# Kernel tuning notes

Hardware: AMD Instinct MI355X
Metric: run time of the kernel (lower is better)

Reference implementation:

```python
import jax, jax.numpy as jnp
import numpy as np

B, S, D, H, E = 4, 1024, 1024, 4096, 8


def setup_inputs() -> dict:
    key = jax.random.key(0)
    ks = jax.random.split(key, 5)
    sd = 1.0 / np.sqrt(D)
    sh = 1.0 / np.sqrt(H)
    x = jax.random.normal(ks[0], (B, S, D), dtype=jnp.float32)
    # stacked expert weights: Linear(D->H), ReLU, Linear(H->D)
    W1 = jax.random.normal(ks[1], (E, D, H), dtype=jnp.float32) * sd
    b1 = jnp.zeros((E, H), dtype=jnp.float32)
    W2 = jax.random.normal(ks[2], (E, H, D), dtype=jnp.float32) * sh
    b2 = jnp.zeros((E, D), dtype=jnp.float32)
    # gate Linear(D->E)
    Wg = jax.random.normal(ks[3], (D, E), dtype=jnp.float32) * sd
    bg = jnp.zeros((E,), dtype=jnp.float32)
    return {"x": x, "W1": W1, "b1": b1, "W2": W2, "b2": b2,
            "Wg": Wg, "bg": bg, "top_k": 2}


def reference(x, W1, b1, W2, b2, Wg, bg, top_k):
    # gating
    gating_scores = jnp.einsum('bsd,de->bse', x, Wg) + bg          # [B,S,E]
    gating_probs = jax.nn.softmax(gating_scores, axis=-1)
    _, top_k_indices = jax.lax.top_k(gating_probs, top_k)          # [B,S,K]
    n_exp = Wg.shape[1]
    # per-token 0/1 mask of selected experts (matches torch sum over k of mask)
    # NOTE: original code multiplies by the binary mask only; top_k_probs are
    # computed but NOT used as combine weights. We reproduce that faithfully.
    sel = jnp.sum(top_k_indices[..., None] == jnp.arange(n_exp), axis=2)  # [B,S,E]
    sel = sel.astype(x.dtype)
    # dense all-experts FFN (as the original does)
    h = jax.nn.relu(jnp.einsum('bsd,edh->bseh', x, W1) + b1)       # [B,S,E,H]
    eo = jnp.einsum('bseh,ehd->bsed', h, W2) + b2                  # [B,S,E,D]
    output = jnp.einsum('bsed,bse->bsd', eo, sel)                  # [B,S,D]
    return (output, gating_scores)
```

## Files before the change

### kernel.cpp

```cpp
#include <hip/hip_runtime.h>
#include <hip/hip_bf16.h>
#include <stdint.h>

#define B_ 4
#define S_ 1024
#define D_ 1024
#define H_ 4096
#define E_ 8
#define T_ (B_*S_)

#define BM 256
#define BN 256
#define BK 64
#define MAXT1 640
#define MAXT2 320

typedef __bf16 bf16x8 __attribute__((ext_vector_type(8)));
typedef float f32x4 __attribute__((ext_vector_type(4)));
typedef unsigned short ushort8 __attribute__((ext_vector_type(8)));

__device__ __forceinline__ unsigned short f2bf(float f) {
  union { float f; uint32_t u; } v; v.f = f;
  uint32_t u = v.u;
  u += 0x7fff + ((u >> 16) & 1);
  return (unsigned short)(u >> 16);
}

__device__ __forceinline__ void gl16(const void* g, void* l) {
  __builtin_amdgcn_global_load_lds(
      (const __attribute__((address_space(1))) void*)g,
      (__attribute__((address_space(3))) void*)l,
      16, 0, 0);
}
#define MEMFENCE asm volatile("" ::: "memory")

__global__ __launch_bounds__(256) void conv_x_kernel(
    const float* __restrict__ x, unsigned short* __restrict__ xb) {
  size_t i = ((size_t)blockIdx.x * 256 + threadIdx.x) * 8;
  const float4* s = (const float4*)(x + i);
  float4 v0 = s[0], v1 = s[1];
  ushort8 w;
  w[0]=f2bf(v0.x); w[1]=f2bf(v0.y); w[2]=f2bf(v0.z); w[3]=f2bf(v0.w);
  w[4]=f2bf(v1.x); w[5]=f2bf(v1.y); w[6]=f2bf(v1.z); w[7]=f2bf(v1.w);
  *(ushort8*)(xb + i) = w;
}

__global__ __launch_bounds__(256) void transpose_conv(
    const float* __restrict__ in, unsigned short* __restrict__ outp,
    int R, int C) {
  __shared__ float tile[64][68];
  const int e = blockIdx.z;
  const size_t eoff = (size_t)e * R * C;
  const int r0 = blockIdx.y * 64, c0 = blockIdx.x * 64;
  const int t = threadIdx.x;
  {
    const int r = t >> 2, cq = (t & 3) * 16;
    const float4* s4 = (const float4*)(in + eoff + (size_t)(r0 + r) * C + (c0 + cq));
#pragma unroll
    for (int i = 0; i < 4; ++i)
      *(float4*)&tile[r][cq + i * 4] = s4[i];
  }
  __syncthreads();
  {
    const int c = t >> 2, r8 = (t & 3) * 16;
    unsigned short* dst = outp + eoff + (size_t)(c0 + c) * R + (r0 + r8);
    ushort8 w0, w1;
#pragma unroll
    for (int j = 0; j < 8; ++j) {
      w0[j] = f2bf(tile[r8 + j][c]);
      w1[j] = f2bf(tile[r8 + 8 + j][c]);
    }
    *(ushort8*)dst = w0;
    *(ushort8*)(dst + 8) = w1;
  }
}

__global__ __launch_bounds__(256) void gating_kernel(
    const float* __restrict__ x, const float* __restrict__ Wg,
    const float* __restrict__ bg, float* __restrict__ scores,
    int* __restrict__ cnt, int* __restrict__ lists) {
  int t = blockIdx.x * 4 + (threadIdx.x >> 6);
  int l = threadIdx.x & 63;
  float acc[E_];
#pragma unroll
  for (int e = 0; e < E_; ++e) acc[e] = 0.f;
  const float* xr = x + (size_t)t * D_;
  for (int k = l; k < D_; k += 64) {
    float xv = xr[k];
    const float4* w = (const float4*)(Wg + (size_t)k * E_);
    float4 w0 = w[0], w1 = w[1];
    acc[0] += xv * w0.x; acc[1] += xv * w0.y; acc[2] += xv * w0.z; acc[3] += xv * w0.w;
    acc[4] += xv * w1.x; acc[5] += xv * w1.y; acc[6] += xv * w1.z; acc[7] += xv * w1.w;
  }
#pragma unroll
  for (int off = 32; off > 0; off >>= 1)
#pragma unroll
    for (int e = 0; e < E_; ++e) acc[e] += __shfl_xor(acc[e], off, 64);
  if (l == 0) {
    float s[E_];
#pragma unroll
    for (int e = 0; e < E_; ++e) {
      s[e] = acc[e] + bg[e];
      scores[(size_t)t * E_ + e] = s[e];
    }
    int i1 = 0; float m1 = -1e30f;
#pragma unroll
    for (int e = 0; e < E_; ++e) if (s[e] > m1) { m1 = s[e]; i1 = e; }
    int i2 = -1; float m2 = -1e30f;
#pragma unroll
    for (int e = 0; e < E_; ++e) if (e != i1 && s[e] > m2) { m2 = s[e]; i2 = e; }
    int p1 = atomicAdd(&cnt[i1], 1); lists[i1 * T_ + p1] = t;
    int p2 = atomicAdd(&cnt[i2], 1); lists[i2 * T_ + p2] = t;
  }
}

__global__ void scan_kernel(const int* __restrict__ cnt, int* __restrict__ off,
                            int* __restrict__ hdr, int* __restrict__ t1tab,
                            int* __restrict__ t2tab) {
  if (threadIdx.x == 0) {
    int o = 0;
    int mtiles[E_];
    for (int e = 0; e < E_; ++e) {
      off[e] = o; o += cnt[e];
      mtiles[e] = (cnt[e] + BM - 1) / BM;
    }
    int n1 = 0;
    for (int e = 0; e < E_; ++e)
      for (int g = 0; g < 4; ++g)
        for (int mt = 0; mt < mtiles[e]; ++mt)
          for (int nl = 0; nl < 4; ++nl)
            t1tab[n1++] = (e << 20) | (mt << 8) | (g * 4 + nl);
    int n2 = 0;
    for (int e = 0; e < E_; ++e)
      for (int sp = 0; sp < 2; ++sp)
        for (int mt = 0; mt < mtiles[e]; ++mt)
          for (int nt = 0; nt < 4; ++nt)
            t2tab[n2++] = (e << 20) | (mt << 8) | (sp << 4) | nt;
    hdr[0] = n1; hdr[1] = n2;
  }
}

template <int LAYER, int SPLITK>
__global__ __launch_bounds__(512, 2) void ffn_gemm(
    const unsigned short* __restrict__ xb,
    const unsigned short* __restrict__ hbuf,
    const unsigned short* __restrict__ WT,
    const float* __restrict__ bias,
    const int* __restrict__ cnt, const int* __restrict__ off,
    const int* __restrict__ lists,
    const int* __restrict__ tab, const int* __restrict__ hdr,
    unsigned short* __restrict__ hout,
    float* __restrict__ out)
{
  constexpr int K = (LAYER == 1) ? D_ : H_;
  constexpr int N = (LAYER == 1) ? H_ : D_;
  constexpr int KS = K / SPLITK;
  constexpr int NT = KS / BK;

  const int ntask = hdr[LAYER - 1];
  const int b = blockIdx.x;
  if (b >= ntask) return;
  const int q = ntask >> 3, r = ntask & 7;
  const int x = b & 7, ii = b >> 3;
  const int task = (x < r ? x * (q + 1) : r * (q + 1) + (x - r) * q) + ii;

  const int ent = tab[task];
  const int e  = ent >> 20;
  const int m0 = ((ent >> 8) & 0xff) * BM;
  const int sp = (ent >> 4) & 3;
  const int n0 = (ent & 15) * BN;
  const int k0 = sp * KS;
  const int count = cnt[e];
  const int oe = off[e];
  const int* lst = lists + e * T_;

  __shared__ unsigned short sA[2][BM * BK];
  __shared__ unsigned short sB[2][BN * BK];

  const int tid  = threadIdx.x;
  const int lane = tid & 63;
  const int wv   = tid >> 6;
  const int wm   = (wv >> 2) * 128;
  const int wn   = (wv & 3) * 64;

  const int srow   = lane >> 3;
  const int schunk = (lane & 7) * 16;
  const int sgoff  = schunk ^ (srow << 4);

  const char* arow[4];
  const char* brow[4];
#pragma unroll
  for (int i = 0; i < 4; ++i) {
    int rr = i * 64 + wv * 8 + srow;
    int gr = m0 + rr;
    if (LAYER == 1) {
      int tok = (gr < count) ? lst[gr] : lst[m0];
      arow[i] = (const char*)(xb + (size_t)tok * K + k0);
    } else {
      int r2 = (gr < count) ? gr : m0;
      arow[i] = (const char*)(hbuf + (size_t)(oe + r2) * K + k0);
    }
    brow[i] = (const char*)(WT + (size_t)e * N * K + (size_t)(n0 + rr) * K + k0);
  }

  auto stage = [&](int buf, int t) {
    const int kb = t * 128;
#pragma unroll
    for (int i = 0; i < 4; ++i)
      gl16(arow[i] + kb + sgoff, (char*)&sA[buf][0] + (i * 64 + wv * 8) * 128);
#pragma unroll
    for (int i = 0; i < 4; ++i)
      gl16(brow[i] + kb + sgoff, (char*)&sB[buf][0] + (i * 64 + wv * 8) * 128);
  };

  const int lrow = lane & 15;
  const int kg   = lane >> 4;
  const int fswz = (lrow & 7) << 4;

  f32x4 acc[8][4];
#pragma unroll
  for (int i = 0; i < 8; ++i)
#pragma unroll
    for (int j = 0; j < 4; ++j) acc[i][j] = (f32x4){0.f, 0.f, 0.f, 0.f};

  stage(0, 0);
  stage(1, 1);
  asm volatile("s_waitcnt vmcnt(8)" ::: "memory");
  __builtin_amdgcn_s_barrier();
  MEMFENCE;

  for (int t = 0; t < NT; ++t) {
    const int buf = t & 1;
    bf16x8 af[8][2], bfm[4][2];
#pragma unroll
    for (int i = 0; i < 8; ++i) {
      const int ra = wm + i * 16 + lrow;
#pragma unroll
      for (int ks = 0; ks < 2; ++ks)
        af[i][ks] = *(const bf16x8*)((const char*)&sA[buf][0] + ra * 128 + ((ks * 64 + kg * 16) ^ fswz));
    }
#pragma unroll
    for (int j = 0; j < 4; ++j) {
      const int rb = wn + j * 16 + lrow;
#pragma unroll
      for (int ks = 0; ks < 2; ++ks)
        bfm[j][ks] = *(const bf16x8*)((const char*)&sB[buf][0] + rb * 128 + ((ks * 64 + kg * 16) ^ fswz));
    }
    MEMFENCE;
    __builtin_amdgcn_s_barrier();
    MEMFENCE;
    if (t + 2 < NT) stage(buf, t + 2);
    __builtin_amdgcn_s_setprio(1);
#pragma unroll
    for (int ks = 0; ks < 2; ++ks)
#pragma unroll
      for (int i = 0; i < 8; ++i)
#pragma unroll
        for (int j = 0; j < 4; ++j)
          acc[i][j] = __builtin_amdgcn_mfma_f32_16x16x32_bf16(af[i][ks], bfm[j][ks], acc[i][j], 0, 0, 0);
    __builtin_amdgcn_s_setprio(0);
    if (t + 2 < NT) {
      asm volatile("s_waitcnt vmcnt(8)" ::: "memory");
    } else if (t + 1 < NT) {
      asm volatile("s_waitcnt vmcnt(0)" ::: "memory");
    }
    MEMFENCE;
    __builtin_amdgcn_s_barrier();
    MEMFENCE;
  }

  const int rbase = 4 * kg;
#pragma unroll
  for (int i = 0; i < 8; ++i) {
#pragma unroll
    for (int r2 = 0; r2 < 4; ++r2) {
      int row  = wm + i * 16 + rbase + r2;
      int grow = m0 + row;
      if (grow < count) {
#pragma unroll
        for (int j = 0; j < 4; ++j) {
          int col  = wn + j * 16 + lrow;
          int gcol = n0 + col;
          float bv = (SPLITK == 1 || sp == 0) ? bias[(size_t)e * N + gcol] : 0.f;
          float v = acc[i][j][r2] + bv;
          if (LAYER == 1) {
            v = v > 0.f ? v : 0.f;
            hout[(size_t)(oe + grow) * H_ + gcol] = f2bf(v);
          } else {
            int tok = lst[grow];
            atomicAdd(&out[(size_t)tok * D_ + gcol], v);
          }
        }
      }
    }
  }
}

extern "C" void kernel_launch(void* const* d_in, const int* in_sizes, int n_in,
                              void* d_out, int out_size, void* d_ws, size_t ws_size,
                              hipStream_t stream) {
  (void)in_sizes; (void)n_in; (void)out_size; (void)ws_size;
  const float* x  = (const float*)d_in[0];
  const float* W1 = (const float*)d_in[1];
  const float* b1 = (const float*)d_in[2];
  const float* W2 = (const float*)d_in[3];
  const float* b2 = (const float*)d_in[4];
  const float* Wg = (const float*)d_in[5];
  const float* bg = (const float*)d_in[6];

  float* out    = (float*)d_out;
  float* scores = out + (size_t)T_ * D_;

  char* ws = (char*)d_ws;
  int* cnt   = (int*)ws;
  int* off   = (int*)(ws + 32);
  int* hdr   = (int*)(ws + 64);
  int* t1tab = (int*)(ws + 128);
  int* t2tab = (int*)(ws + 128 + 4 * MAXT1);
  int* lists = (int*)(ws + 8192);
  unsigned short* xb   = (unsigned short*)(ws + 8192 + 131072);
  unsigned short* hbuf = (unsigned short*)(ws + 8192 + 131072 + 8388608);
  unsigned short* WT   = (unsigned short*)(ws + 8192 + 131072 + 8388608 + 67108864);

  hipMemsetAsync(out, 0, (size_t)T_ * D_ * sizeof(float), stream);
  hipMemsetAsync(cnt, 0, 64, stream);

  conv_x_kernel<<<(T_ * D_) / (256 * 8), 256, 0, stream>>>(x, xb);
  gating_kernel<<<T_ / 4, 256, 0, stream>>>(x, Wg, bg, scores, cnt, lists);
  scan_kernel<<<1, 64, 0, stream>>>(cnt, off, hdr, t1tab, t2tab);

  transpose_conv<<<dim3(H_ / 64, D_ / 64, E_), 256, 0, stream>>>(W1, WT, D_, H_);
  ffn_gemm<1, 1><<<MAXT1, 512, 0, stream>>>(
      xb, hbuf, WT, b1, cnt, off, lists, t1tab, hdr, hbuf, nullptr);

  transpose_conv<<<dim3(D_ / 64, H_ / 64, E_), 256, 0, stream>>>(W2, WT, H_, D_);
  ffn_gemm<2, 2><<<MAXT2, 512, 0, stream>>>(
      xb, hbuf, WT, b2, cnt, off, lists, t2tab, hdr, nullptr, out);
}
```

Baseline: 512.7 us.

## Shrink GEMM tiles to 128x128 with 256 threads and single-buffered LDS loop

The grouped expert GEMMs move from 256x256 tiles with 512 threads and a double-buffered, hand-scheduled LDS pipeline to 128x128 tiles with 256 threads. The new loop loads one LDS buffer per k-step and synchronises with plain __syncthreads. The task tables and workspace offsets are regenerated for the finer tiling, which gives many more blocks and three blocks per CU. This should improve load balance and occupancy across ragged per-expert token counts, but it gives up software prefetch overlap and per-tile data reuse, so each tile does more global/LDS traffic and more barrier stalls.

```diff
diff --git a/kernel.cpp b/kernel.cpp
--- a/kernel.cpp
+++ b/kernel.cpp
@@ -9,11 +9,10 @@
 #define E_ 8
 #define T_ (B_*S_)
 
-#define BM 256
-#define BN 256
+#define GBM 128
 #define BK 64
-#define MAXT1 640
-#define MAXT2 320
+#define MAXT1 2432
+#define MAXT2 1280
 
 typedef __bf16 bf16x8 __attribute__((ext_vector_type(8)));
 typedef float f32x4 __attribute__((ext_vector_type(4)));
@@ -32,7 +31,6 @@
       (__attribute__((address_space(3))) void*)l,
       16, 0, 0);
 }
-#define MEMFENCE asm volatile("" ::: "memory")
 
 __global__ __launch_bounds__(256) void conv_x_kernel(
     const float* __restrict__ x, unsigned short* __restrict__ xb) {
@@ -122,26 +120,25 @@
     int mtiles[E_];
     for (int e = 0; e < E_; ++e) {
       off[e] = o; o += cnt[e];
-      mtiles[e] = (cnt[e] + BM - 1) / BM;
+      mtiles[e] = (cnt[e] + GBM - 1) / GBM;
     }
     int n1 = 0;
     for (int e = 0; e < E_; ++e)
-      for (int g = 0; g < 4; ++g)
+      for (int nt = 0; nt < H_ / GBM; ++nt)
         for (int mt = 0; mt < mtiles[e]; ++mt)
-          for (int nl = 0; nl < 4; ++nl)
-            t1tab[n1++] = (e << 20) | (mt << 8) | (g * 4 + nl);
+          t1tab[n1++] = (e << 16) | (mt << 8) | nt;
     int n2 = 0;
     for (int e = 0; e < E_; ++e)
       for (int sp = 0; sp < 2; ++sp)
-        for (int mt = 0; mt < mtiles[e]; ++mt)
-          for (int nt = 0; nt < 4; ++nt)
-            t2tab[n2++] = (e << 20) | (mt << 8) | (sp << 4) | nt;
+        for (int nt = 0; nt < D_ / GBM; ++nt)
+          for (int mt = 0; mt < mtiles[e]; ++mt)
+            t2tab[n2++] = (e << 16) | (mt << 8) | (sp << 6) | nt;
     hdr[0] = n1; hdr[1] = n2;
   }
 }
 
 template <int LAYER, int SPLITK>
-__global__ __launch_bounds__(512, 2) void ffn_gemm(
+__global__ __launch_bounds__(256, 3) void ffn_gemm(
     const unsigned short* __restrict__ xb,
     const unsigned short* __restrict__ hbuf,
     const unsigned short* __restrict__ WT,
@@ -165,23 +162,23 @@
   const int task = (x < r ? x * (q + 1) : r * (q + 1) + (x - r) * q) + ii;
 
   const int ent = tab[task];
-  const int e  = ent >> 20;
-  const int m0 = ((ent >> 8) & 0xff) * BM;
-  const int sp = (ent >> 4) & 3;
-  const int n0 = (ent & 15) * BN;
+  const int e  = ent >> 16;
+  const int m0 = ((ent >> 8) & 0xff) * GBM;
+  const int sp = (ent >> 6) & 3;
+  const int n0 = (ent & 63) * GBM;
   const int k0 = sp * KS;
   const int count = cnt[e];
   const int oe = off[e];
   const int* lst = lists + e * T_;
 
-  __shared__ unsigned short sA[2][BM * BK];
-  __shared__ unsigned short sB[2][BN * BK];
+  __shared__ unsigned short sA[GBM * BK];
+  __shared__ unsigned short sB[GBM * BK];
 
   const int tid  = threadIdx.x;
   const int lane = tid & 63;
   const int wv   = tid >> 6;
-  const int wm   = (wv >> 2) * 128;
-  const int wn   = (wv & 3) * 64;
+  const int wm   = (wv >> 1) * 64;
+  const int wn   = (wv & 1) * 64;
 
   const int srow   = lane >> 3;
   const int schunk = (lane & 7) * 16;
@@ -191,7 +188,7 @@
   const char* brow[4];
 #pragma unroll
   for (int i = 0; i < 4; ++i) {
-    int rr = i * 64 + wv * 8 + srow;
+    int rr = i * 32 + wv * 8 + srow;
     int gr = m0 + rr;
     if (LAYER == 1) {
       int tok = (gr < count) ? lst[gr] : lst[m0];
@@ -203,75 +200,47 @@
     brow[i] = (const char*)(WT + (size_t)e * N * K + (size_t)(n0 + rr) * K + k0);
   }
 
-  auto stage = [&](int buf, int t) {
-    const int kb = t * 128;
-#pragma unroll
-    for (int i = 0; i < 4; ++i)
-      gl16(arow[i] + kb + sgoff, (char*)&sA[buf][0] + (i * 64 + wv * 8) * 128);
-#pragma unroll
-    for (int i = 0; i < 4; ++i)
-      gl16(brow[i] + kb + sgoff, (char*)&sB[buf][0] + (i * 64 + wv * 8) * 128);
-  };
-
   const int lrow = lane & 15;
   const int kg   = lane >> 4;
   const int fswz = (lrow & 7) << 4;
 
-  f32x4 acc[8][4];
-#pragma unroll
-  for (int i = 0; i < 8; ++i)
+  f32x4 acc[4][4];
+#pragma unroll
+  for (int i = 0; i < 4; ++i)
 #pragma unroll
     for (int j = 0; j < 4; ++j) acc[i][j] = (f32x4){0.f, 0.f, 0.f, 0.f};
 
-  stage(0, 0);
-  stage(1, 1);
-  asm volatile("s_waitcnt vmcnt(8)" ::: "memory");
-  __builtin_amdgcn_s_barrier();
-  MEMFENCE;
-
+#pragma unroll 1
   for (int t = 0; t < NT; ++t) {
-    const int buf = t & 1;
-    bf16x8 af[8][2], bfm[4][2];
-#pragma unroll
-    for (int i = 0; i < 8; ++i) {
-      const int ra = wm + i * 16 + lrow;
-#pragma unroll
-      for (int ks = 0; ks < 2; ++ks)
-        af[i][ks] = *(const bf16x8*)((const char*)&sA[buf][0] + ra * 128 + ((ks * 64 + kg * 16) ^ fswz));
-    }
-#pragma unroll
-    for (int j = 0; j < 4; ++j) {
-      const int rb = wn + j * 16 + lrow;
-#pragma unroll
-      for (int ks = 0; ks < 2; ++ks)
-        bfm[j][ks] = *(const bf16x8*)((const char*)&sB[buf][0] + rb * 128 + ((ks * 64 + kg * 16) ^ fswz));
-    }
-    MEMFENCE;
-    __builtin_amdgcn_s_barrier();
-    MEMFENCE;
-    if (t + 2 < NT) stage(buf, t + 2);
-    __builtin_amdgcn_s_setprio(1);
-#pragma unroll
-    for (int ks = 0; ks < 2; ++ks)
-#pragma unroll
-      for (int i = 0; i < 8; ++i)
+    const int kb = t * 128;
+#pragma unroll
+    for (int i = 0; i < 4; ++i)
+      gl16(arow[i] + kb + sgoff, (char*)sA + (i * 32 + wv * 8) * 128);
+#pragma unroll
+    for (int i = 0; i < 4; ++i)
+      gl16(brow[i] + kb + sgoff, (char*)sB + (i * 32 + wv * 8) * 128);
+    __syncthreads();
+#pragma unroll
+    for (int ks = 0; ks < 2; ++ks) {
+      bf16x8 af[4], bfm[4];
+      const int kbyte = ks * 64 + kg * 16;
+#pragma unroll
+      for (int i = 0; i < 4; ++i) {
+        af[i]  = *(const bf16x8*)((const char*)sA + (wm + i * 16 + lrow) * 128 + (kbyte ^ fswz));
+        bfm[i] = *(const bf16x8*)((const char*)sB + (wn + i * 16 + lrow) * 128 + (kbyte ^ fswz));
+      }
+#pragma unroll
+      for (int i = 0; i < 4; ++i)
 #pragma unroll
         for (int j = 0; j < 4; ++j)
-          acc[i][j] = __builtin_amdgcn_mfma_f32_16x16x32_bf16(af[i][ks], bfm[j][ks], acc[i][j], 0, 0, 0);
-    __builtin_amdgcn_s_setprio(0);
-    if (t + 2 < NT) {
-      asm volatile("s_waitcnt vmcnt(8)" ::: "memory");
-    } else if (t + 1 < NT) {
-      asm volatile("s_waitcnt vmcnt(0)" ::: "memory");
-    }
-    MEMFENCE;
-    __builtin_amdgcn_s_barrier();
-    MEMFENCE;
+          acc[i][j] = __builtin_amdgcn_mfma_f32_16x16x32_bf16(af[i], bfm[j], acc[i][j], 0, 0, 0);
+    }
+    __syncthreads();
   }
 
   const int rbase = 4 * kg;
 #pragma unroll
-  for (int i = 0; i < 8; ++i) {
+  for (int i = 0; i < 4; ++i) {
 #pragma unroll
     for (int r2 = 0; r2 < 4; ++r2) {
       int row  = wm + i * 16 + rbase + r2;
@@ -316,11 +285,11 @@
   int* off   = (int*)(ws + 32);
   int* hdr   = (int*)(ws + 64);
   int* t1tab = (int*)(ws + 128);
-  int* t2tab = (int*)(ws + 128 + 4 * MAXT1);
-  int* lists = (int*)(ws + 8192);
-  unsigned short* xb   = (unsigned short*)(ws + 8192 + 131072);
-  unsigned short* hbuf = (unsigned short*)(ws + 8192 + 131072 + 8388608);
-  unsigned short* WT   = (unsigned short*)(ws + 8192 + 131072 + 8388608 + 67108864);
+  int* t2tab = (int*)(ws + 10240);
+  int* lists = (int*)(ws + 16384);
+  unsigned short* xb   = (unsigned short*)(ws + 16384 + 131072);
+  unsigned short* hbuf = (unsigned short*)(ws + 16384 + 131072 + 8388608);
+  unsigned short* WT   = (unsigned short*)(ws + 16384 + 131072 + 8388608 + 67108864);
 
   hipMemsetAsync(out, 0, (size_t)T_ * D_ * sizeof(float), stream);
   hipMemsetAsync(cnt, 0, 64, stream);
@@ -330,10 +299,10 @@
   scan_kernel<<<1, 64, 0, stream>>>(cnt, off, hdr, t1tab, t2tab);
 
   transpose_conv<<<dim3(H_ / 64, D_ / 64, E_), 256, 0, stream>>>(W1, WT, D_, H_);
-  ffn_gemm<1, 1><<<MAXT1, 512, 0, stream>>>(
+  ffn_gemm<1, 1><<<MAXT1, 256, 0, stream>>>(
       xb, hbuf, WT, b1, cnt, off, lists, t1tab, hdr, hbuf, nullptr);
 
   transpose_conv<<<dim3(D_ / 64, H_ / 64, E_), 256, 0, stream>>>(W2, WT, H_, D_);
-  ffn_gemm<2, 2><<<MAXT2, 512, 0, stream>>>(
+  ffn_gemm<2, 2><<<MAXT2, 256, 0, stream>>>(
       xb, hbuf, WT, b2, cnt, off, lists, t2tab, hdr, nullptr, out);
 }
```

After: 496.9 us. 3.1% less time.
